# Performance work log

Measured on AMD Instinct MI355X. Metric: run time of the kernel, lower is better.

Reference implementation:

```python
import jax, jax.numpy as jnp
import numpy as np

GROUP = 16  # 4-bit quantization group size along in_features
LN_EPS = 1e-5


def dequant4bit(q, s):
    # q: [O, I] int32 values in [0, 15]; s: [O, I//GROUP] per-group absmax scales
    O, I = q.shape
    w = q.astype(jnp.float32) * (2.0 / 15.0) - 1.0          # map to [-1, 1]
    w = w.reshape(O, I // GROUP, GROUP) * s[:, :, None]      # per-group scale
    return w.reshape(O, I)


def qlora_linear(x, q, s, b, A, B):
    # base 4-bit dequantized matmul + bias
    w = dequant4bit(q, s)                                    # [O, I]
    base = x @ w.T + b                                       # [N, O]
    # LoRA low-rank delta; scaling = lora_alpha/lora_dim = 1.0
    delta = (x @ A.T) @ B.T                                  # [N, r] @ [r, O]
    return base + delta


def layernorm(x, g, b):
    m = jnp.mean(x, axis=-1, keepdims=True)
    v = jnp.mean((x - m) ** 2, axis=-1, keepdims=True)
    return (x - m) * jax.lax.rsqrt(v + LN_EPS) * g + b


def setup_inputs() -> dict:
    key = jax.random.key(0)
    ks = jax.random.split(key, 6)
    N, D, R, L, NB = 16384, 1024, 32, 18, 6  # tokens, dim, lora rank, num linears, num blocks
    x = jax.random.normal(ks[0], (N, D), dtype=jnp.float32)
    qw = jax.random.randint(ks[1], (L, D, D), 0, 16, dtype=jnp.int32)
    scales = jax.random.uniform(ks[2], (L, D, D // GROUP), dtype=jnp.float32) * 0.1
    bias = jax.random.normal(ks[3], (L, D), dtype=jnp.float32) * 0.02
    lora_A = jax.random.normal(ks[4], (L, R, D), dtype=jnp.float32) * 0.02
    lora_B = jax.random.normal(ks[5], (L, D, R), dtype=jnp.float32) * 0.02
    ln_g = jnp.ones((NB - 1, D), dtype=jnp.float32)
    ln_b = jnp.zeros((NB - 1, D), dtype=jnp.float32)
    return {"x": x, "qw": qw, "scales": scales, "bias": bias,
            "lora_A": lora_A, "lora_B": lora_B, "ln_g": ln_g, "ln_b": ln_b}


def reference(x, qw, scales, bias, lora_A, lora_B, ln_g, ln_b):
    n_blocks = 6
    for blk in range(n_blocks):
        h = x
        for j in range(3):
            li = 3 * blk + j
            h = qlora_linear(h, qw[li], scales[li], bias[li], lora_A[li], lora_B[li])
            if j < 2:
                h = jax.nn.relu(h)
        x = h + x  # residual
        if blk < n_blocks - 1:
            x = layernorm(x, ln_g[blk], ln_b[blk])
    return x
```

## Files before the change

kernel.cpp:

```cpp
#include <hip/hip_runtime.h>
#include <cstdint>


#define NTOK 16384
#define DIM  1024
#define KP   1088
#define RLORA 32
#define NLIN 18
#define NBLK 6

typedef unsigned short u16;
typedef __attribute__((ext_vector_type(8))) short short8;
typedef __attribute__((ext_vector_type(4))) float f32x4;

__device__ __forceinline__ u16 f2bf(float f) {
  uint32_t u = __float_as_uint(f);
  u += 0x7fffu + ((u >> 16) & 1u);
  return (u16)(u >> 16);
}
__device__ __forceinline__ float bf2f(u16 h) {
  return __uint_as_float(((uint32_t)h) << 16);
}
__device__ __forceinline__ void split_bf(float f, u16& h, u16& l) {
  h = f2bf(f);
  l = f2bf(f - bf2f(h));
}

__device__ __forceinline__ void gld16(const void* g, void* lds) {
  __builtin_amdgcn_global_load_lds(
      (const __attribute__((address_space(1))) uint32_t*)g,
      (__attribute__((address_space(3))) uint32_t*)lds, 16, 0, 0);
}


__global__ void pack_w_k(const int* __restrict__ qw, const float* __restrict__ sc,
                         const float* __restrict__ lb,
                         u16* __restrict__ Wh, u16* __restrict__ Wl) {
  const int idx = blockIdx.x * 256 + threadIdx.x;
  if (idx >= 1024 * (KP / 16)) return;
  const int g = idx % (KP / 16);
  const int o = idx / (KP / 16);
  u16 h[16], l[16];
  if (g < 64) {
    const int* q = qw + (size_t)o * 1024 + g * 16;
    const float s = sc[(size_t)o * 64 + g];
#pragma unroll
    for (int j = 0; j < 16; ++j) {
      float w = ((float)q[j] * (2.0f / 15.0f) - 1.0f) * s;
      split_bf(w, h[j], l[j]);
    }
  } else if (g < 66) {
    const float* B = lb + (size_t)o * RLORA + (g - 64) * 16;
#pragma unroll
    for (int j = 0; j < 16; ++j) split_bf(B[j], h[j], l[j]);
  } else {
#pragma unroll
    for (int j = 0; j < 16; ++j) { h[j] = 0; l[j] = 0; }
  }
  u16* wh = Wh + (size_t)o * KP + g * 16;
  u16* wl = Wl + (size_t)o * KP + g * 16;
#pragma unroll
  for (int j = 0; j < 16; ++j) { wh[j] = h[j]; wl[j] = l[j]; }
}

__global__ void pack_a_k(const float* __restrict__ la,
                         u16* __restrict__ Ah, u16* __restrict__ Al) {
  const int idx = blockIdx.x * 256 + threadIdx.x;
  if (idx >= NLIN * RLORA * (KP / 16)) return;
  const int g = idx % (KP / 16);
  const int rem = idx / (KP / 16);
  const int r = rem % RLORA, li = rem / RLORA;
  u16 h[16], l[16];
  if (g < 64) {
    const float* a = la + ((size_t)li * RLORA + r) * 1024 + g * 16;
#pragma unroll
    for (int j = 0; j < 16; ++j) split_bf(a[j], h[j], l[j]);
  } else {
#pragma unroll
    for (int j = 0; j < 16; ++j) { h[j] = 0; l[j] = 0; }
  }
  u16* ph = Ah + ((size_t)li * RLORA + r) * KP + g * 16;
  u16* pl = Al + ((size_t)li * RLORA + r) * KP + g * 16;
#pragma unroll
  for (int j = 0; j < 16; ++j) { ph[j] = h[j]; pl[j] = l[j]; }
}

__global__ void pack_x_k(const float* __restrict__ x,
                         u16* __restrict__ aAh, u16* __restrict__ aAl,
                         u16* __restrict__ aBh, u16* __restrict__ aBl) {
  const int idx = blockIdx.x * 256 + threadIdx.x;
  if (idx >= NTOK * (KP / 16)) return;
  const int g = idx % (KP / 16);
  const int n = idx / (KP / 16);
  const size_t dofs = (size_t)n * KP + g * 16;
  if (g < 64) {
    const float* xp = x + (size_t)n * DIM + g * 16;
#pragma unroll
    for (int j = 0; j < 16; ++j) {
      u16 h, l;
      split_bf(xp[j], h, l);
      aAh[dofs + j] = h; aAl[dofs + j] = l;
    }
  } else {
#pragma unroll
    for (int j = 0; j < 16; ++j) {
      aAh[dofs + j] = 0; aAl[dofs + j] = 0;
      aBh[dofs + j] = 0; aBl[dofs + j] = 0;
    }
  }
}

__global__ __launch_bounds__(256, 4) void t_k(
    u16* __restrict__ Xh, u16* __restrict__ Xl,
    const u16* __restrict__ LAh, const u16* __restrict__ LAl) {
  __shared__ __align__(16) u16 sXh[128 * 64], sXl[128 * 64];
  const int tid = threadIdx.x;
  const int lane = tid & 63, wave = tid >> 6;
  const int row0 = blockIdx.x * 128;

  f32x4 acc[2][2];
#pragma unroll
  for (int i = 0; i < 2; ++i)
#pragma unroll
    for (int j = 0; j < 2; ++j) acc[i][j] = {0.f, 0.f, 0.f, 0.f};

  const int sr = tid >> 3;
  const int ss = ((tid & 7) ^ (sr & 7)) * 8;
  const size_t xoff = (size_t)(row0 + sr) * KP + ss;
  const int arow = wave * 32 + (lane & 15);
  const int sl = lane >> 4, sx = lane & 7;

  for (int ks = 0; ks < 16; ++ks) {
    const int kofs = ks * 64;
#pragma unroll
    for (int r = 0; r < 4; ++r) {
      const size_t go = (size_t)(r * 32) * KP + kofs;
      const int lo = wave * 512 + r * 2048;
      gld16(Xh + xoff + go, &sXh[lo]);
      gld16(Xl + xoff + go, &sXl[lo]);
    }
    __syncthreads();
#pragma unroll
    for (int kk = 0; kk < 2; ++kk) {
      const int so = ((kk * 4 + sl) ^ sx) * 8;
      const int o0 = arow * 64 + so;
      const int o1 = (arow + 16) * 64 + so;
      short8 a0h = *(const short8*)&sXh[o0];
      short8 a0l = *(const short8*)&sXl[o0];
      short8 a1h = *(const short8*)&sXh[o1];
      short8 a1l = *(const short8*)&sXl[o1];
#pragma unroll
      for (int ni = 0; ni < 2; ++ni) {
        const int ar = ni * 16 + (lane & 15);
        const int ac = kofs + kk * 32 + sl * 8;
        short8 bh = *(const short8*)&LAh[(size_t)ar * KP + ac];
        short8 bl = *(const short8*)&LAl[(size_t)ar * KP + ac];
        f32x4 c = acc[0][ni];
        c = __builtin_amdgcn_mfma_f32_16x16x32_bf16(a0h, bl, c, 0, 0, 0);
        c = __builtin_amdgcn_mfma_f32_16x16x32_bf16(a0l, bh, c, 0, 0, 0);
        c = __builtin_amdgcn_mfma_f32_16x16x32_bf16(a0h, bh, c, 0, 0, 0);
        acc[0][ni] = c;
        c = acc[1][ni];
        c = __builtin_amdgcn_mfma_f32_16x16x32_bf16(a1h, bl, c, 0, 0, 0);
        c = __builtin_amdgcn_mfma_f32_16x16x32_bf16(a1l, bh, c, 0, 0, 0);
        c = __builtin_amdgcn_mfma_f32_16x16x32_bf16(a1h, bh, c, 0, 0, 0);
        acc[1][ni] = c;
      }
    }
    __syncthreads();
  }
  const int crow0 = row0 + wave * 32 + (lane >> 4) * 4;
#pragma unroll
  for (int ni = 0; ni < 2; ++ni) {
    const int col = DIM + ni * 16 + (lane & 15);
#pragma unroll
    for (int mi = 0; mi < 2; ++mi)
#pragma unroll
      for (int r = 0; r < 4; ++r) {
        const int rw = crow0 + mi * 16 + r;
        u16 h, l;
        split_bf(acc[mi][ni][r], h, l);
        Xh[(size_t)rw * KP + col] = h;
        Xl[(size_t)rw * KP + col] = l;
      }
  }
}

template <int MODE>
__global__ __launch_bounds__(256, 2) void gemm_k(
    const u16* __restrict__ Xh, const u16* __restrict__ Xl,
    const u16* __restrict__ Wh, const u16* __restrict__ Wl,
    const float* __restrict__ bias, const float* __restrict__ resid,
    float* __restrict__ outf, u16* __restrict__ Oh, u16* __restrict__ Ol) {
  __shared__ __align__(16) u16 sXh[128 * 64], sXl[128 * 64];
  __shared__ __align__(16) u16 sWh[128 * 64], sWl[128 * 64];
  const int tid = threadIdx.x;
  const int lane = tid & 63, wave = tid >> 6;
  const int wr = wave >> 1, wc = wave & 1;
  const int row0 = blockIdx.x * 128, col0 = blockIdx.y * 128;

  f32x4 acc[4][4];
#pragma unroll
  for (int i = 0; i < 4; ++i)
#pragma unroll
    for (int j = 0; j < 4; ++j) acc[i][j] = {0.f, 0.f, 0.f, 0.f};

  const int sr = tid >> 3;
  const int ss = ((tid & 7) ^ (sr & 7)) * 8;
  const size_t xoff = (size_t)(row0 + sr) * KP + ss;
  const size_t woff = (size_t)(col0 + sr) * KP + ss;

  const int arow = wr * 64 + (lane & 15);
  const int brow = wc * 64 + (lane & 15);
  const int sl = lane >> 4, sx = lane & 7;

  for (int ks = 0; ks < KP / 64; ++ks) {
    const int kofs = ks * 64;
#pragma unroll
    for (int r = 0; r < 4; ++r) {
      const size_t go = (size_t)(r * 32) * KP + kofs;
      const int lo = wave * 512 + r * 2048;
      gld16(Xh + xoff + go, &sXh[lo]);
      gld16(Xl + xoff + go, &sXl[lo]);
      gld16(Wh + woff + go, &sWh[lo]);
      gld16(Wl + woff + go, &sWl[lo]);
    }
    __syncthreads();
#pragma unroll
    for (int kk = 0; kk < 2; ++kk) {
      const int so = ((kk * 4 + sl) ^ sx) * 8;
      short8 ah[4], am[4], bh[4], bm[4];
#pragma unroll
      for (int mi = 0; mi < 4; ++mi) {
        const int off = (arow + mi * 16) * 64 + so;
        ah[mi] = *(const short8*)&sXh[off];
        am[mi] = *(const short8*)&sXl[off];
      }
#pragma unroll
      for (int ni = 0; ni < 4; ++ni) {
        const int off = (brow + ni * 16) * 64 + so;
        bh[ni] = *(const short8*)&sWh[off];
        bm[ni] = *(const short8*)&sWl[off];
      }
#pragma unroll
      for (int mi = 0; mi < 4; ++mi)
#pragma unroll
        for (int ni = 0; ni < 4; ++ni) {
          f32x4 c = acc[mi][ni];
          c = __builtin_amdgcn_mfma_f32_16x16x32_bf16(ah[mi], bm[ni], c, 0, 0, 0);
          c = __builtin_amdgcn_mfma_f32_16x16x32_bf16(am[mi], bh[ni], c, 0, 0, 0);
          c = __builtin_amdgcn_mfma_f32_16x16x32_bf16(ah[mi], bh[ni], c, 0, 0, 0);
          acc[mi][ni] = c;
        }
    }
    __syncthreads();
  }

  const int crow0 = row0 + wr * 64 + (lane >> 4) * 4;
  const int ccol0 = col0 + wc * 64 + (lane & 15);
#pragma unroll
  for (int ni = 0; ni < 4; ++ni) {
    const int col = ccol0 + ni * 16;
    const float bv = bias[col];
#pragma unroll
    for (int mi = 0; mi < 4; ++mi) {
#pragma unroll
      for (int r = 0; r < 4; ++r) {
        const int rw = crow0 + mi * 16 + r;
        float v = acc[mi][ni][r] + bv;
        if (MODE == 0) {
          v = fmaxf(v, 0.f);
          u16 h, l;
          split_bf(v, h, l);
          Oh[(size_t)rw * KP + col] = h;
          Ol[(size_t)rw * KP + col] = l;
        } else {
          v += resid[(size_t)rw * DIM + col];
          outf[(size_t)rw * DIM + col] = v;
        }
      }
    }
  }
}

__global__ __launch_bounds__(256) void ln_k(
    const float* __restrict__ y, const float* __restrict__ g,
    const float* __restrict__ b, float* __restrict__ ro,
    u16* __restrict__ Oh, u16* __restrict__ Ol) {
  const int row = blockIdx.x, tid = threadIdx.x;
  const int lane = tid & 63, wave = tid >> 6;
  __shared__ float r1[4], r2[4];
  const float4 v = ((const float4*)(y + (size_t)row * DIM))[tid];
  float s = v.x + v.y + v.z + v.w;
#pragma unroll
  for (int o = 32; o > 0; o >>= 1) s += __shfl_down(s, o);
  if (lane == 0) r1[wave] = s;
  __syncthreads();
  const float mean = (r1[0] + r1[1] + r1[2] + r1[3]) * (1.0f / DIM);
  const float d0 = v.x - mean, d1 = v.y - mean, d2 = v.z - mean, d3 = v.w - mean;
  float q = d0 * d0 + d1 * d1 + d2 * d2 + d3 * d3;
#pragma unroll
  for (int o = 32; o > 0; o >>= 1) q += __shfl_down(q, o);
  if (lane == 0) r2[wave] = q;
  __syncthreads();
  const float var = (r2[0] + r2[1] + r2[2] + r2[3]) * (1.0f / DIM);
  const float rs = rsqrtf(var + 1e-5f);
  const float4 gv = ((const float4*)g)[tid];
  const float4 bv = ((const float4*)b)[tid];
  const float o0 = d0 * rs * gv.x + bv.x;
  const float o1 = d1 * rs * gv.y + bv.y;
  const float o2 = d2 * rs * gv.z + bv.z;
  const float o3 = d3 * rs * gv.w + bv.w;
  ((float4*)(ro + (size_t)row * DIM))[tid] = make_float4(o0, o1, o2, o3);
  u16 h0, l0, h1, l1, h2, l2, h3, l3;
  split_bf(o0, h0, l0); split_bf(o1, h1, l1);
  split_bf(o2, h2, l2); split_bf(o3, h3, l3);
  ushort4 hh; hh.x = h0; hh.y = h1; hh.z = h2; hh.w = h3;
  ushort4 ll; ll.x = l0; ll.y = l1; ll.z = l2; ll.w = l3;
  *(ushort4*)&Oh[(size_t)row * KP + tid * 4] = hh;
  *(ushort4*)&Ol[(size_t)row * KP + tid * 4] = ll;
}

extern "C" void kernel_launch(void* const* d_in, const int* in_sizes, int n_in,
                              void* d_out, int out_size, void* d_ws, size_t ws_size,
                              hipStream_t stream) {
  const float* x      = (const float*)d_in[0];
  const int*   qw     = (const int*)d_in[1];
  const float* scales = (const float*)d_in[2];
  const float* bias   = (const float*)d_in[3];
  const float* lora_A = (const float*)d_in[4];
  const float* lora_B = (const float*)d_in[5];
  const float* ln_g   = (const float*)d_in[6];
  const float* ln_b   = (const float*)d_in[7];

  char* p = (char*)d_ws;
  auto carve = [&](size_t bytes) {
    char* r = p;
    p += (bytes + 255) & ~(size_t)255;
    return (void*)r;
  };
  u16* Wh  = (u16*)carve((size_t)1024 * KP * 2);
  u16* Wl  = (u16*)carve((size_t)1024 * KP * 2);
  u16* Ah  = (u16*)carve((size_t)NLIN * RLORA * KP * 2);
  u16* Al  = (u16*)carve((size_t)NLIN * RLORA * KP * 2);
  u16* aAh = (u16*)carve((size_t)NTOK * KP * 2);
  u16* aAl = (u16*)carve((size_t)NTOK * KP * 2);
  u16* aBh = (u16*)carve((size_t)NTOK * KP * 2);
  u16* aBl = (u16*)carve((size_t)NTOK * KP * 2);
  float* residb = (float*)carve((size_t)NTOK * DIM * 4);
  float* ybuf   = (float*)d_out;

  {
    const int tot = NLIN * RLORA * (KP / 16);
    pack_a_k<<<(tot + 255) / 256, 256, 0, stream>>>(lora_A, Ah, Al);
  }
  {
    const int tot = NTOK * (KP / 16);
    pack_x_k<<<(tot + 255) / 256, 256, 0, stream>>>(x, aAh, aAl, aBh, aBl);
  }

  u16 *inH = aAh, *inL = aAl, *outH = aBh, *outL = aBl;
  const float* resid = x;
  const int wtot = 1024 * (KP / 16);
  for (int blk = 0; blk < NBLK; ++blk) {
    for (int j = 0; j < 3; ++j) {
      const int li = 3 * blk + j;
      pack_w_k<<<(wtot + 255) / 256, 256, 0, stream>>>(
          qw + (size_t)li * DIM * DIM, scales + (size_t)li * DIM * (DIM / 16),
          lora_B + (size_t)li * DIM * RLORA, Wh, Wl);
      t_k<<<NTOK / 128, 256, 0, stream>>>(
          inH, inL, Ah + (size_t)li * RLORA * KP, Al + (size_t)li * RLORA * KP);
      const float* lb = bias + (size_t)li * DIM;
      dim3 grid(NTOK / 128, DIM / 128);
      if (j < 2) {
        gemm_k<0><<<grid, 256, 0, stream>>>(inH, inL, Wh, Wl, lb,
                                            nullptr, nullptr, outH, outL);
        u16* t;
        t = inH; inH = outH; outH = t;
        t = inL; inL = outL; outL = t;
      } else {
        gemm_k<1><<<grid, 256, 0, stream>>>(inH, inL, Wh, Wl, lb,
                                            resid, ybuf, nullptr, nullptr);
        if (blk < NBLK - 1) {
          ln_k<<<NTOK, 256, 0, stream>>>(ybuf, ln_g + (size_t)blk * DIM,
                                         ln_b + (size_t)blk * DIM, residb,
                                         outH, outL);
          resid = residb;
          u16* t;
          t = inH; inH = outH; outH = t;
          t = inL; inL = outL; outL = t;
        }
      }
    }
  }
  (void)in_sizes; (void)n_in; (void)out_size; (void)ws_size;
}
```

Before: 2.920 ms.

## Concatenate hi/lo split operands along K and use 256x256 pipelined GEMM

Activations and weights are re-laid out so the hi and lo bf16 halves are concatenated along K (X=[h|l], W=[h|l|h]), which turns the three-MFMA split-bf16 product into one long GEMM with K=3264. The main GEMM becomes a 512-thread, 256x256-tile kernel with double-buffered LDS, staggered global-to-LDS prefetch, s_setprio around MFMA phases and a swizzled block order. The LoRA t_k kernel likewise uses the concatenated layout with double buffering. The intent is more data reuse per tile and better overlap of loads with MFMAs. The cost is higher register and LDS pressure. The LoRA intermediate is now stored only as hi bf16, dropping its lo part, so precision is slightly reduced.

```diff
diff --git a/kernel.cpp b/kernel.cpp
--- a/kernel.cpp
+++ b/kernel.cpp
@@ -5,6 +5,9 @@
 #define NTOK 16384
 #define DIM  1024
 #define KP   1088
+#define KX   2176
+#define KC   3264
+#define NSTEP 51
 #define RLORA 32
 #define NLIN 18
 #define NBLK 6
@@ -25,255 +28,303 @@
   h = f2bf(f);
   l = f2bf(f - bf2f(h));
 }
-
 __device__ __forceinline__ void gld16(const void* g, void* lds) {
   __builtin_amdgcn_global_load_lds(
       (const __attribute__((address_space(1))) uint32_t*)g,
       (__attribute__((address_space(3))) uint32_t*)lds, 16, 0, 0);
 }
 
-
 __global__ void pack_w_k(const int* __restrict__ qw, const float* __restrict__ sc,
-                         const float* __restrict__ lb,
-                         u16* __restrict__ Wh, u16* __restrict__ Wl) {
+                         const float* __restrict__ lb, u16* __restrict__ Wc) {
   const int idx = blockIdx.x * 256 + threadIdx.x;
-  if (idx >= 1024 * (KP / 16)) return;
-  const int g = idx % (KP / 16);
-  const int o = idx / (KP / 16);
-  u16 h[16], l[16];
-  if (g < 64) {
+  if (idx >= 1024 * (KC / 16)) return;
+  const int c = idx % (KC / 16);
+  const int o = idx / (KC / 16);
+  int kind = 4, g = 0;
+  if      (c < 64)  { kind = 0; g = c; }
+  else if (c < 66)  { kind = 2; g = c - 64; }
+  else if (c < 68)  { kind = 4; }
+  else if (c < 132) { kind = 1; g = c - 68; }
+  else if (c < 134) { kind = 3; g = c - 132; }
+  else if (c < 136) { kind = 4; }
+  else if (c < 200) { kind = 0; g = c - 136; }
+  else if (c < 202) { kind = 2; g = c - 200; }
+  u16 out[16];
+  if (kind == 0 || kind == 1) {
     const int* q = qw + (size_t)o * 1024 + g * 16;
     const float s = sc[(size_t)o * 64 + g];
 #pragma unroll
     for (int j = 0; j < 16; ++j) {
       float w = ((float)q[j] * (2.0f / 15.0f) - 1.0f) * s;
-      split_bf(w, h[j], l[j]);
-    }
-  } else if (g < 66) {
-    const float* B = lb + (size_t)o * RLORA + (g - 64) * 16;
-#pragma unroll
-    for (int j = 0; j < 16; ++j) split_bf(B[j], h[j], l[j]);
+      u16 h, l; split_bf(w, h, l);
+      out[j] = (kind == 0) ? h : l;
+    }
+  } else if (kind == 2 || kind == 3) {
+    const float* B = lb + (size_t)o * RLORA + g * 16;
+#pragma unroll
+    for (int j = 0; j < 16; ++j) {
+      u16 h, l; split_bf(B[j], h, l);
+      out[j] = (kind == 2) ? h : l;
+    }
   } else {
 #pragma unroll
-    for (int j = 0; j < 16; ++j) { h[j] = 0; l[j] = 0; }
-  }
-  u16* wh = Wh + (size_t)o * KP + g * 16;
-  u16* wl = Wl + (size_t)o * KP + g * 16;
-#pragma unroll
-  for (int j = 0; j < 16; ++j) { wh[j] = h[j]; wl[j] = l[j]; }
-}
-
-__global__ void pack_a_k(const float* __restrict__ la,
-                         u16* __restrict__ Ah, u16* __restrict__ Al) {
+    for (int j = 0; j < 16; ++j) out[j] = 0;
+  }
+  u16* w = Wc + (size_t)o * KC + c * 16;
+#pragma unroll
+  for (int j = 0; j < 16; ++j) w[j] = out[j];
+}
+
+__global__ void pack_a_k(const float* __restrict__ la, u16* __restrict__ Ac) {
   const int idx = blockIdx.x * 256 + threadIdx.x;
-  if (idx >= NLIN * RLORA * (KP / 16)) return;
-  const int g = idx % (KP / 16);
-  const int rem = idx / (KP / 16);
-  const int r = rem % RLORA, li = rem / RLORA;
-  u16 h[16], l[16];
-  if (g < 64) {
-    const float* a = la + ((size_t)li * RLORA + r) * 1024 + g * 16;
-#pragma unroll
-    for (int j = 0; j < 16; ++j) split_bf(a[j], h[j], l[j]);
+  if (idx >= NLIN * RLORA * (KX / 16)) return;
+  const int c = idx % (KX / 16);
+  const int rr = idx / (KX / 16);
+  u16 out[16];
+  int kind = 2, g = 0;
+  if (c < 64) { kind = 0; g = c; }
+  else if (c >= 68 && c < 132) { kind = 1; g = c - 68; }
+  if (kind < 2) {
+    const float* a = la + (size_t)rr * 1024 + g * 16;
+#pragma unroll
+    for (int j = 0; j < 16; ++j) {
+      u16 h, l; split_bf(a[j], h, l);
+      out[j] = (kind == 0) ? h : l;
+    }
   } else {
 #pragma unroll
-    for (int j = 0; j < 16; ++j) { h[j] = 0; l[j] = 0; }
-  }
-  u16* ph = Ah + ((size_t)li * RLORA + r) * KP + g * 16;
-  u16* pl = Al + ((size_t)li * RLORA + r) * KP + g * 16;
-#pragma unroll
-  for (int j = 0; j < 16; ++j) { ph[j] = h[j]; pl[j] = l[j]; }
+    for (int j = 0; j < 16; ++j) out[j] = 0;
+  }
+  u16* p = Ac + (size_t)rr * KX + c * 16;
+#pragma unroll
+  for (int j = 0; j < 16; ++j) p[j] = out[j];
 }
 
 __global__ void pack_x_k(const float* __restrict__ x,
-                         u16* __restrict__ aAh, u16* __restrict__ aAl,
-                         u16* __restrict__ aBh, u16* __restrict__ aBl) {
+                         u16* __restrict__ aA, u16* __restrict__ aB) {
   const int idx = blockIdx.x * 256 + threadIdx.x;
-  if (idx >= NTOK * (KP / 16)) return;
-  const int g = idx % (KP / 16);
-  const int n = idx / (KP / 16);
-  const size_t dofs = (size_t)n * KP + g * 16;
-  if (g < 64) {
-    const float* xp = x + (size_t)n * DIM + g * 16;
+  if (idx >= NTOK * 68) return;
+  const int c = idx % 68;
+  const int n = idx / 68;
+  const size_t base = (size_t)n * KX;
+  if (c < 64) {
+    const float* xp = x + (size_t)n * DIM + c * 16;
 #pragma unroll
     for (int j = 0; j < 16; ++j) {
-      u16 h, l;
-      split_bf(xp[j], h, l);
-      aAh[dofs + j] = h; aAl[dofs + j] = l;
+      u16 h, l; split_bf(xp[j], h, l);
+      aA[base + c * 16 + j] = h;
+      aA[base + KP + c * 16 + j] = l;
     }
   } else {
 #pragma unroll
     for (int j = 0; j < 16; ++j) {
-      aAh[dofs + j] = 0; aAl[dofs + j] = 0;
-      aBh[dofs + j] = 0; aBl[dofs + j] = 0;
+      aA[base + c * 16 + j] = 0;      aA[base + KP + c * 16 + j] = 0;
+      aB[base + c * 16 + j] = 0;      aB[base + KP + c * 16 + j] = 0;
     }
   }
 }
 
 __global__ __launch_bounds__(256, 4) void t_k(
-    u16* __restrict__ Xh, u16* __restrict__ Xl,
-    const u16* __restrict__ LAh, const u16* __restrict__ LAl) {
-  __shared__ __align__(16) u16 sXh[128 * 64], sXl[128 * 64];
+    u16* __restrict__ X, const u16* __restrict__ Ac) {
+  __shared__ __align__(16) u16 sX[2][128 * 64];
+  const int tid = threadIdx.x, lane = tid & 63, wave = tid >> 6;
+  const int row0 = blockIdx.x * 128;
+  const int srow = tid >> 3;
+  const int lslot = ((tid & 7) ^ (srow & 7)) * 8;
+  const int fr = lane & 15, sl = lane >> 4, sx = lane & 7;
+
+  f32x4 acc[2][2];
+#pragma unroll
+  for (int i = 0; i < 2; ++i)
+#pragma unroll
+    for (int j = 0; j < 2; ++j) acc[i][j] = {0.f, 0.f, 0.f, 0.f};
+
+  auto stage = [&](int buf, int s) {
+    const int xb = (s < 17 ? s : s - 17) * 64;
+#pragma unroll
+    for (int i = 0; i < 4; ++i)
+      gld16(X + (size_t)(row0 + i * 32 + srow) * KX + xb + lslot,
+            &sX[buf][i * 2048 + wave * 512]);
+  };
+  stage(0, 0);
+  for (int t = 0; t < 34; ++t) {
+    const int c = t & 1;
+    if (t + 1 < 34) {
+      stage(c ^ 1, t + 1);
+      asm volatile("s_waitcnt vmcnt(4)" ::: "memory");
+    } else {
+      asm volatile("s_waitcnt vmcnt(0)" ::: "memory");
+    }
+    __builtin_amdgcn_s_barrier();
+    short8 av[2][2], bv[2][2];
+#pragma unroll
+    for (int mi = 0; mi < 2; ++mi)
+#pragma unroll
+      for (int kk = 0; kk < 2; ++kk) {
+        const int row = wave * 32 + mi * 16 + fr;
+        av[mi][kk] = *(const short8*)&sX[c][row * 64 + (((kk * 4 + sl) ^ sx)) * 8];
+      }
+#pragma unroll
+    for (int ni = 0; ni < 2; ++ni)
+#pragma unroll
+      for (int kk = 0; kk < 2; ++kk) {
+        const int ar = ni * 16 + fr;
+        bv[ni][kk] = *(const short8*)&Ac[(size_t)ar * KX + t * 64 + kk * 32 + sl * 8];
+      }
+#pragma unroll
+    for (int mi = 0; mi < 2; ++mi)
+#pragma unroll
+      for (int ni = 0; ni < 2; ++ni)
+#pragma unroll
+        for (int kk = 0; kk < 2; ++kk)
+          acc[mi][ni] = __builtin_amdgcn_mfma_f32_16x16x32_bf16(
+              av[mi][kk], bv[ni][kk], acc[mi][ni], 0, 0, 0);
+    __builtin_amdgcn_s_barrier();
+  }
+  const int crow0 = row0 + wave * 32 + (lane >> 4) * 4;
+#pragma unroll
+  for (int ni = 0; ni < 2; ++ni) {
+    const int col = DIM + ni * 16 + fr;
+#pragma unroll
+    for (int mi = 0; mi < 2; ++mi)
+#pragma unroll
+      for (int r = 0; r < 4; ++r)
+        X[(size_t)(crow0 + mi * 16 + r) * KX + col] = f2bf(acc[mi][ni][r]);
+  }
+}
+
+#define READ_A(Q)                                                           \
+  short8 aa0[2], aa1[2];                                                    \
+  {                                                                         \
+    const int r0 = (wr * 128 + ((Q) * 2 + 0) * 16 + fr) * 64;               \
+    const int r1 = (wr * 128 + ((Q) * 2 + 1) * 16 + fr) * 64;               \
+    aa0[0] = *(const short8*)&sA[c][r0 + ((0 + sl) ^ sx) * 8];              \
+    aa0[1] = *(const short8*)&sA[c][r0 + ((4 + sl) ^ sx) * 8];              \
+    aa1[0] = *(const short8*)&sA[c][r1 + ((0 + sl) ^ sx) * 8];              \
+    aa1[1] = *(const short8*)&sA[c][r1 + ((4 + sl) ^ sx) * 8];              \
+  }
+
+#define PHASE_TAIL(Q)                                                       \
+  __builtin_amdgcn_s_barrier();                                             \
+  asm volatile("s_waitcnt lgkmcnt(0)" ::: "memory");                        \
+  __builtin_amdgcn_s_setprio(1);                                            \
+  _Pragma("unroll")                                                         \
+  for (int kk = 0; kk < 2; ++kk) {                                          \
+    _Pragma("unroll")                                                       \
+    for (int ni = 0; ni < 4; ++ni) {                                        \
+      acc[(Q) * 2 + 0][ni] = __builtin_amdgcn_mfma_f32_16x16x32_bf16(       \
+          aa0[kk], b[ni][kk], acc[(Q) * 2 + 0][ni], 0, 0, 0);               \
+      acc[(Q) * 2 + 1][ni] = __builtin_amdgcn_mfma_f32_16x16x32_bf16(       \
+          aa1[kk], b[ni][kk], acc[(Q) * 2 + 1][ni], 0, 0, 0);               \
+    }                                                                       \
+  }                                                                         \
+  __builtin_amdgcn_s_setprio(0);                                            \
+  __builtin_amdgcn_s_barrier();
+
+template <int MODE>
+__global__ __launch_bounds__(512, 2) void gemm8_k(
+    const u16* __restrict__ X, const u16* __restrict__ W,
+    const float* __restrict__ bias, const float* __restrict__ resid,
+    float* __restrict__ outf, u16* __restrict__ O) {
+  __shared__ __align__(16) u16 sA[2][256 * 64];
+  __shared__ __align__(16) u16 sB[2][256 * 64];
   const int tid = threadIdx.x;
   const int lane = tid & 63, wave = tid >> 6;
-  const int row0 = blockIdx.x * 128;
-
-  f32x4 acc[2][2];
-#pragma unroll
-  for (int i = 0; i < 2; ++i)
-#pragma unroll
-    for (int j = 0; j < 2; ++j) acc[i][j] = {0.f, 0.f, 0.f, 0.f};
-
-  const int sr = tid >> 3;
-  const int ss = ((tid & 7) ^ (sr & 7)) * 8;
-  const size_t xoff = (size_t)(row0 + sr) * KP + ss;
-  const int arow = wave * 32 + (lane & 15);
-  const int sl = lane >> 4, sx = lane & 7;
-
-  for (int ks = 0; ks < 16; ++ks) {
-    const int kofs = ks * 64;
-#pragma unroll
-    for (int r = 0; r < 4; ++r) {
-      const size_t go = (size_t)(r * 32) * KP + kofs;
-      const int lo = wave * 512 + r * 2048;
-      gld16(Xh + xoff + go, &sXh[lo]);
-      gld16(Xl + xoff + go, &sXl[lo]);
-    }
-    __syncthreads();
-#pragma unroll
-    for (int kk = 0; kk < 2; ++kk) {
-      const int so = ((kk * 4 + sl) ^ sx) * 8;
-      const int o0 = arow * 64 + so;
-      const int o1 = (arow + 16) * 64 + so;
-      short8 a0h = *(const short8*)&sXh[o0];
-      short8 a0l = *(const short8*)&sXl[o0];
-      short8 a1h = *(const short8*)&sXh[o1];
-      short8 a1l = *(const short8*)&sXl[o1];
-#pragma unroll
-      for (int ni = 0; ni < 2; ++ni) {
-        const int ar = ni * 16 + (lane & 15);
-        const int ac = kofs + kk * 32 + sl * 8;
-        short8 bh = *(const short8*)&LAh[(size_t)ar * KP + ac];
-        short8 bl = *(const short8*)&LAl[(size_t)ar * KP + ac];
-        f32x4 c = acc[0][ni];
-        c = __builtin_amdgcn_mfma_f32_16x16x32_bf16(a0h, bl, c, 0, 0, 0);
-        c = __builtin_amdgcn_mfma_f32_16x16x32_bf16(a0l, bh, c, 0, 0, 0);
-        c = __builtin_amdgcn_mfma_f32_16x16x32_bf16(a0h, bh, c, 0, 0, 0);
-        acc[0][ni] = c;
-        c = acc[1][ni];
-        c = __builtin_amdgcn_mfma_f32_16x16x32_bf16(a1h, bl, c, 0, 0, 0);
-        c = __builtin_amdgcn_mfma_f32_16x16x32_bf16(a1l, bh, c, 0, 0, 0);
-        c = __builtin_amdgcn_mfma_f32_16x16x32_bf16(a1h, bh, c, 0, 0, 0);
-        acc[1][ni] = c;
+  const int wr = wave >> 2, wc = wave & 3;
+
+  const int flat = blockIdx.y * 64 + blockIdx.x;
+  const int fl2 = (flat & 7) * 32 + (flat >> 3);
+  const int row0 = (fl2 & 63) * 256;
+  const int col0 = (fl2 >> 6) * 256;
+
+  const int srow = tid >> 3;
+  const int lslot = ((tid & 7) ^ (srow & 7)) * 8;
+  const int fr = lane & 15, sl = lane >> 4, sx = lane & 7;
+
+  f32x4 acc[8][4];
+#pragma unroll
+  for (int i = 0; i < 8; ++i)
+#pragma unroll
+    for (int j = 0; j < 4; ++j) acc[i][j] = {0.f, 0.f, 0.f, 0.f};
+
+  auto xbase = [](int s) {
+    return s < 17 ? s * 64 : (s < 34 ? (s - 17) * 64 : KP + (s - 34) * 64);
+  };
+  auto stX = [&](int buf, int s, int i) {
+    gld16(X + (size_t)(row0 + i * 64 + srow) * KX + xbase(s) + lslot,
+          &sA[buf][i * 4096 + wave * 512]);
+  };
+  auto stW = [&](int buf, int s, int i) {
+    gld16(W + (size_t)(col0 + i * 64 + srow) * KC + s * 64 + lslot,
+          &sB[buf][i * 4096 + wave * 512]);
+  };
+
+#pragma unroll
+  for (int i = 0; i < 4; ++i) stX(0, 0, i);
+#pragma unroll
+  for (int i = 0; i < 4; ++i) stW(0, 0, i);
+#pragma unroll
+  for (int i = 0; i < 4; ++i) stW(1, 1, i);
+  stX(1, 1, 0);
+  stX(1, 1, 2);
+  asm volatile("s_waitcnt vmcnt(6)" ::: "memory");
+  __builtin_amdgcn_s_barrier();
+
+  for (int t = 0; t < NSTEP; ++t) {
+    const int c = t & 1;
+    const bool h1 = (t + 1 < NSTEP), h2 = (t + 2 < NSTEP);
+    short8 b[4][2];
+#pragma unroll
+    for (int ni = 0; ni < 4; ++ni) {
+      const int row = (wc * 64 + ni * 16 + fr) * 64;
+#pragma unroll
+      for (int kk = 0; kk < 2; ++kk)
+        b[ni][kk] = *(const short8*)&sB[c][row + ((kk * 4 + sl) ^ sx) * 8];
+    }
+    {
+      READ_A(0)
+      if (h1) { stX(c ^ 1, t + 1, 1); stX(c ^ 1, t + 1, 3); }
+      PHASE_TAIL(0)
+    }
+    {
+      READ_A(1)
+      if (h2) { stW(c, t + 2, 0); stW(c, t + 2, 1); }
+      PHASE_TAIL(1)
+    }
+    {
+      READ_A(2)
+      if (h2) { stW(c, t + 2, 2); stW(c, t + 2, 3); stX(c, t + 2, 0); }
+      PHASE_TAIL(2)
+    }
+    {
+      READ_A(3)
+      if (h2) {
+        stX(c, t + 2, 2);
+        asm volatile("s_waitcnt vmcnt(6)" ::: "memory");
+      } else if (h1) {
+        asm volatile("s_waitcnt vmcnt(0)" ::: "memory");
       }
-    }
-    __syncthreads();
-  }
-  const int crow0 = row0 + wave * 32 + (lane >> 4) * 4;
-#pragma unroll
-  for (int ni = 0; ni < 2; ++ni) {
-    const int col = DIM + ni * 16 + (lane & 15);
-#pragma unroll
-    for (int mi = 0; mi < 2; ++mi)
+      PHASE_TAIL(3)
+    }
+  }
+
+  const int crow0 = row0 + wr * 128 + (lane >> 4) * 4;
+  const int ccolb = col0 + wc * 64 + fr;
+#pragma unroll
+  for (int ni = 0; ni < 4; ++ni) {
+    const int col = ccolb + ni * 16;
+    const float bvv = bias[col];
+#pragma unroll
+    for (int mi = 0; mi < 8; ++mi) {
 #pragma unroll
       for (int r = 0; r < 4; ++r) {
         const int rw = crow0 + mi * 16 + r;
-        u16 h, l;
-        split_bf(acc[mi][ni][r], h, l);
-        Xh[(size_t)rw * KP + col] = h;
-        Xl[(size_t)rw * KP + col] = l;
-      }
-  }
-}
-
-template <int MODE>
-__global__ __launch_bounds__(256, 2) void gemm_k(
-    const u16* __restrict__ Xh, const u16* __restrict__ Xl,
-    const u16* __restrict__ Wh, const u16* __restrict__ Wl,
-    const float* __restrict__ bias, const float* __restrict__ resid,
-    float* __restrict__ outf, u16* __restrict__ Oh, u16* __restrict__ Ol) {
-  __shared__ __align__(16) u16 sXh[128 * 64], sXl[128 * 64];
-  __shared__ __align__(16) u16 sWh[128 * 64], sWl[128 * 64];
-  const int tid = threadIdx.x;
-  const int lane = tid & 63, wave = tid >> 6;
-  const int wr = wave >> 1, wc = wave & 1;
-  const int row0 = blockIdx.x * 128, col0 = blockIdx.y * 128;
-
-  f32x4 acc[4][4];
-#pragma unroll
-  for (int i = 0; i < 4; ++i)
-#pragma unroll
-    for (int j = 0; j < 4; ++j) acc[i][j] = {0.f, 0.f, 0.f, 0.f};
-
-  const int sr = tid >> 3;
-  const int ss = ((tid & 7) ^ (sr & 7)) * 8;
-  const size_t xoff = (size_t)(row0 + sr) * KP + ss;
-  const size_t woff = (size_t)(col0 + sr) * KP + ss;
-
-  const int arow = wr * 64 + (lane & 15);
-  const int brow = wc * 64 + (lane & 15);
-  const int sl = lane >> 4, sx = lane & 7;
-
-  for (int ks = 0; ks < KP / 64; ++ks) {
-    const int kofs = ks * 64;
-#pragma unroll
-    for (int r = 0; r < 4; ++r) {
-      const size_t go = (size_t)(r * 32) * KP + kofs;
-      const int lo = wave * 512 + r * 2048;
-      gld16(Xh + xoff + go, &sXh[lo]);
-      gld16(Xl + xoff + go, &sXl[lo]);
-      gld16(Wh + woff + go, &sWh[lo]);
-      gld16(Wl + woff + go, &sWl[lo]);
-    }
-    __syncthreads();
-#pragma unroll
-    for (int kk = 0; kk < 2; ++kk) {
-      const int so = ((kk * 4 + sl) ^ sx) * 8;
-      short8 ah[4], am[4], bh[4], bm[4];
-#pragma unroll
-      for (int mi = 0; mi < 4; ++mi) {
-        const int off = (arow + mi * 16) * 64 + so;
-        ah[mi] = *(const short8*)&sXh[off];
-        am[mi] = *(const short8*)&sXl[off];
-      }
-#pragma unroll
-      for (int ni = 0; ni < 4; ++ni) {
-        const int off = (brow + ni * 16) * 64 + so;
-        bh[ni] = *(const short8*)&sWh[off];
-        bm[ni] = *(const short8*)&sWl[off];
-      }
-#pragma unroll
-      for (int mi = 0; mi < 4; ++mi)
-#pragma unroll
-        for (int ni = 0; ni < 4; ++ni) {
-          f32x4 c = acc[mi][ni];
-          c = __builtin_amdgcn_mfma_f32_16x16x32_bf16(ah[mi], bm[ni], c, 0, 0, 0);
-          c = __builtin_amdgcn_mfma_f32_16x16x32_bf16(am[mi], bh[ni], c, 0, 0, 0);
-          c = __builtin_amdgcn_mfma_f32_16x16x32_bf16(ah[mi], bh[ni], c, 0, 0, 0);
-          acc[mi][ni] = c;
-        }
-    }
-    __syncthreads();
-  }
-
-  const int crow0 = row0 + wr * 64 + (lane >> 4) * 4;
-  const int ccol0 = col0 + wc * 64 + (lane & 15);
-#pragma unroll
-  for (int ni = 0; ni < 4; ++ni) {
-    const int col = ccol0 + ni * 16;
-    const float bv = bias[col];
-#pragma unroll
-    for (int mi = 0; mi < 4; ++mi) {
-#pragma unroll
-      for (int r = 0; r < 4; ++r) {
-        const int rw = crow0 + mi * 16 + r;
-        float v = acc[mi][ni][r] + bv;
+        float v = acc[mi][ni][r] + bvv;
         if (MODE == 0) {
           v = fmaxf(v, 0.f);
-          u16 h, l;
-          split_bf(v, h, l);
-          Oh[(size_t)rw * KP + col] = h;
-          Ol[(size_t)rw * KP + col] = l;
+          u16 h, l; split_bf(v, h, l);
+          O[(size_t)rw * KX + col] = h;
+          O[(size_t)rw * KX + KP + col] = l;
         } else {
           v += resid[(size_t)rw * DIM + col];
           outf[(size_t)rw * DIM + col] = v;
@@ -285,8 +336,7 @@
 
 __global__ __launch_bounds__(256) void ln_k(
     const float* __restrict__ y, const float* __restrict__ g,
-    const float* __restrict__ b, float* __restrict__ ro,
-    u16* __restrict__ Oh, u16* __restrict__ Ol) {
+    const float* __restrict__ b, float* __restrict__ ro, u16* __restrict__ O) {
   const int row = blockIdx.x, tid = threadIdx.x;
   const int lane = tid & 63, wave = tid >> 6;
   __shared__ float r1[4], r2[4];
@@ -317,8 +367,8 @@
   split_bf(o2, h2, l2); split_bf(o3, h3, l3);
   ushort4 hh; hh.x = h0; hh.y = h1; hh.z = h2; hh.w = h3;
   ushort4 ll; ll.x = l0; ll.y = l1; ll.z = l2; ll.w = l3;
-  *(ushort4*)&Oh[(size_t)row * KP + tid * 4] = hh;
-  *(ushort4*)&Ol[(size_t)row * KP + tid * 4] = ll;
+  *(ushort4*)&O[(size_t)row * KX + tid * 4] = hh;
+  *(ushort4*)&O[(size_t)row * KX + KP + tid * 4] = ll;
 }
 
 extern "C" void kernel_launch(void* const* d_in, const int* in_sizes, int n_in,
@@ -339,56 +389,44 @@
     p += (bytes + 255) & ~(size_t)255;
     return (void*)r;
   };
-  u16* Wh  = (u16*)carve((size_t)1024 * KP * 2);
-  u16* Wl  = (u16*)carve((size_t)1024 * KP * 2);
-  u16* Ah  = (u16*)carve((size_t)NLIN * RLORA * KP * 2);
-  u16* Al  = (u16*)carve((size_t)NLIN * RLORA * KP * 2);
-  u16* aAh = (u16*)carve((size_t)NTOK * KP * 2);
-  u16* aAl = (u16*)carve((size_t)NTOK * KP * 2);
-  u16* aBh = (u16*)carve((size_t)NTOK * KP * 2);
-  u16* aBl = (u16*)carve((size_t)NTOK * KP * 2);
+  u16* Wc  = (u16*)carve((size_t)1024 * KC * 2);
+  u16* Ac  = (u16*)carve((size_t)NLIN * RLORA * KX * 2);
+  u16* aA  = (u16*)carve((size_t)NTOK * KX * 2);
+  u16* aB  = (u16*)carve((size_t)NTOK * KX * 2);
   float* residb = (float*)carve((size_t)NTOK * DIM * 4);
   float* ybuf   = (float*)d_out;
 
   {
-    const int tot = NLIN * RLORA * (KP / 16);
-    pack_a_k<<<(tot + 255) / 256, 256, 0, stream>>>(lora_A, Ah, Al);
+    const int tot = NLIN * RLORA * (KX / 16);
+    pack_a_k<<<(tot + 255) / 256, 256, 0, stream>>>(lora_A, Ac);
   }
   {
-    const int tot = NTOK * (KP / 16);
-    pack_x_k<<<(tot + 255) / 256, 256, 0, stream>>>(x, aAh, aAl, aBh, aBl);
-  }
-
-  u16 *inH = aAh, *inL = aAl, *outH = aBh, *outL = aBl;
+    const int tot = NTOK * 68;
+    pack_x_k<<<(tot + 255) / 256, 256, 0, stream>>>(x, aA, aB);
+  }
+
+  u16 *inA = aA, *outA = aB;
   const float* resid = x;
-  const int wtot = 1024 * (KP / 16);
+  const int wtot = 1024 * (KC / 16);
+  dim3 grid(64, 4);
   for (int blk = 0; blk < NBLK; ++blk) {
     for (int j = 0; j < 3; ++j) {
       const int li = 3 * blk + j;
       pack_w_k<<<(wtot + 255) / 256, 256, 0, stream>>>(
           qw + (size_t)li * DIM * DIM, scales + (size_t)li * DIM * (DIM / 16),
-          lora_B + (size_t)li * DIM * RLORA, Wh, Wl);
-      t_k<<<NTOK / 128, 256, 0, stream>>>(
-          inH, inL, Ah + (size_t)li * RLORA * KP, Al + (size_t)li * RLORA * KP);
+          lora_B + (size_t)li * DIM * RLORA, Wc);
+      t_k<<<NTOK / 128, 256, 0, stream>>>(inA, Ac + (size_t)li * RLORA * KX);
       const float* lb = bias + (size_t)li * DIM;
-      dim3 grid(NTOK / 128, DIM / 128);
       if (j < 2) {
-        gemm_k<0><<<grid, 256, 0, stream>>>(inH, inL, Wh, Wl, lb,
-                                            nullptr, nullptr, outH, outL);
-        u16* t;
-        t = inH; inH = outH; outH = t;
-        t = inL; inL = outL; outL = t;
+        gemm8_k<0><<<grid, 512, 0, stream>>>(inA, Wc, lb, nullptr, nullptr, outA);
+        u16* tswp = inA; inA = outA; outA = tswp;
       } else {
-        gemm_k<1><<<grid, 256, 0, stream>>>(inH, inL, Wh, Wl, lb,
-                                            resid, ybuf, nullptr, nullptr);
+        gemm8_k<1><<<grid, 512, 0, stream>>>(inA, Wc, lb, resid, ybuf, nullptr);
         if (blk < NBLK - 1) {
           ln_k<<<NTOK, 256, 0, stream>>>(ybuf, ln_g + (size_t)blk * DIM,
-                                         ln_b + (size_t)blk * DIM, residb,
-                                         outH, outL);
+                                         ln_b + (size_t)blk * DIM, residb, outA);
           resid = residb;
-          u16* t;
-          t = inH; inH = outH; outH = t;
-          t = inL; inL = outL; outL = t;
+          u16* tswp = inA; inA = outA; outA = tswp;
         }
       }
     }
```

Result: slower. 3.680 ms (+26.0%).

## Slim LoRA projection kernel to bf16-hi input and remap GEMM blocks per XCD

Applied to the files above, without the earlier changes.

The LoRA down-projection kernel now loads only the high bf16 half of the activations, uses 64-row tiles with two MFMAs per step instead of three, and writes only the high part of the projected result. This cuts shared memory, traffic and MFMA work in that kernel, at some cost in precision in the LoRA path. The main GEMM remaps its flat block index so blocks on the same XCD share row panels and all column tiles, aiming for better L2 reuse. The pack_a index math is also simplified.

```diff
diff --git a/kernel.cpp b/kernel.cpp
--- a/kernel.cpp
+++ b/kernel.cpp
@@ -69,18 +69,17 @@
   if (idx >= NLIN * RLORA * (KP / 16)) return;
   const int g = idx % (KP / 16);
   const int rem = idx / (KP / 16);
-  const int r = rem % RLORA, li = rem / RLORA;
   u16 h[16], l[16];
   if (g < 64) {
-    const float* a = la + ((size_t)li * RLORA + r) * 1024 + g * 16;
+    const float* a = la + (size_t)rem * 1024 + g * 16;
 #pragma unroll
     for (int j = 0; j < 16; ++j) split_bf(a[j], h[j], l[j]);
   } else {
 #pragma unroll
     for (int j = 0; j < 16; ++j) { h[j] = 0; l[j] = 0; }
   }
-  u16* ph = Ah + ((size_t)li * RLORA + r) * KP + g * 16;
-  u16* pl = Al + ((size_t)li * RLORA + r) * KP + g * 16;
+  u16* ph = Ah + (size_t)rem * KP + g * 16;
+  u16* pl = Al + (size_t)rem * KP + g * 16;
 #pragma unroll
   for (int j = 0; j < 16; ++j) { ph[j] = h[j]; pl[j] = l[j]; }
 }
@@ -111,78 +110,52 @@
 }
 
 __global__ __launch_bounds__(256, 4) void t_k(
-    u16* __restrict__ Xh, u16* __restrict__ Xl,
-    const u16* __restrict__ LAh, const u16* __restrict__ LAl) {
-  __shared__ __align__(16) u16 sXh[128 * 64], sXl[128 * 64];
-  const int tid = threadIdx.x;
-  const int lane = tid & 63, wave = tid >> 6;
-  const int row0 = blockIdx.x * 128;
-
-  f32x4 acc[2][2];
-#pragma unroll
-  for (int i = 0; i < 2; ++i)
-#pragma unroll
-    for (int j = 0; j < 2; ++j) acc[i][j] = {0.f, 0.f, 0.f, 0.f};
-
-  const int sr = tid >> 3;
-  const int ss = ((tid & 7) ^ (sr & 7)) * 8;
-  const size_t xoff = (size_t)(row0 + sr) * KP + ss;
-  const int arow = wave * 32 + (lane & 15);
-  const int sl = lane >> 4, sx = lane & 7;
-
-  for (int ks = 0; ks < 16; ++ks) {
-    const int kofs = ks * 64;
-#pragma unroll
-    for (int r = 0; r < 4; ++r) {
-      const size_t go = (size_t)(r * 32) * KP + kofs;
-      const int lo = wave * 512 + r * 2048;
-      gld16(Xh + xoff + go, &sXh[lo]);
-      gld16(Xl + xoff + go, &sXl[lo]);
-    }
+    u16* __restrict__ Xh, const u16* __restrict__ LAh,
+    const u16* __restrict__ LAl) {
+  __shared__ __align__(16) u16 sX[64 * 64];
+  const int tid = threadIdx.x, lane = tid & 63, wave = tid >> 6;
+  const int row0 = blockIdx.x * 64;
+  const int fr = lane & 15, sl = lane >> 4;
+  const int xr = tid >> 3, xs = tid & 7;
+
+  f32x4 acc[2];
+  acc[0] = {0.f, 0.f, 0.f, 0.f};
+  acc[1] = {0.f, 0.f, 0.f, 0.f};
+
+  for (int t = 0; t < 16; ++t) {
+    const int kofs = t * 64;
+    gld16(Xh + (size_t)(row0 + xr) * KP + kofs + (xs ^ (xr & 7)) * 8,
+          &sX[tid * 8]);
+    gld16(Xh + (size_t)(row0 + 32 + xr) * KP + kofs + (xs ^ (xr & 7)) * 8,
+          &sX[2048 + tid * 8]);
     __syncthreads();
+    short8 a[2];
 #pragma unroll
     for (int kk = 0; kk < 2; ++kk) {
-      const int so = ((kk * 4 + sl) ^ sx) * 8;
-      const int o0 = arow * 64 + so;
-      const int o1 = (arow + 16) * 64 + so;
-      short8 a0h = *(const short8*)&sXh[o0];
-      short8 a0l = *(const short8*)&sXl[o0];
-      short8 a1h = *(const short8*)&sXh[o1];
-      short8 a1l = *(const short8*)&sXl[o1];
-#pragma unroll
-      for (int ni = 0; ni < 2; ++ni) {
-        const int ar = ni * 16 + (lane & 15);
+      const int arow = wave * 16 + fr;
+      a[kk] = *(const short8*)&sX[arow * 64 + (((kk * 4 + sl) ^ (fr & 7))) * 8];
+    }
+#pragma unroll
+    for (int n = 0; n < 2; ++n) {
+      const int ar = n * 16 + fr;
+#pragma unroll
+      for (int kk = 0; kk < 2; ++kk) {
         const int ac = kofs + kk * 32 + sl * 8;
         short8 bh = *(const short8*)&LAh[(size_t)ar * KP + ac];
         short8 bl = *(const short8*)&LAl[(size_t)ar * KP + ac];
-        f32x4 c = acc[0][ni];
-        c = __builtin_amdgcn_mfma_f32_16x16x32_bf16(a0h, bl, c, 0, 0, 0);
-        c = __builtin_amdgcn_mfma_f32_16x16x32_bf16(a0l, bh, c, 0, 0, 0);
-        c = __builtin_amdgcn_mfma_f32_16x16x32_bf16(a0h, bh, c, 0, 0, 0);
-        acc[0][ni] = c;
-        c = acc[1][ni];
-        c = __builtin_amdgcn_mfma_f32_16x16x32_bf16(a1h, bl, c, 0, 0, 0);
-        c = __builtin_amdgcn_mfma_f32_16x16x32_bf16(a1l, bh, c, 0, 0, 0);
-        c = __builtin_amdgcn_mfma_f32_16x16x32_bf16(a1h, bh, c, 0, 0, 0);
-        acc[1][ni] = c;
+        acc[n] = __builtin_amdgcn_mfma_f32_16x16x32_bf16(a[kk], bh, acc[n], 0, 0, 0);
+        acc[n] = __builtin_amdgcn_mfma_f32_16x16x32_bf16(a[kk], bl, acc[n], 0, 0, 0);
       }
     }
     __syncthreads();
   }
-  const int crow0 = row0 + wave * 32 + (lane >> 4) * 4;
-#pragma unroll
-  for (int ni = 0; ni < 2; ++ni) {
-    const int col = DIM + ni * 16 + (lane & 15);
-#pragma unroll
-    for (int mi = 0; mi < 2; ++mi)
-#pragma unroll
-      for (int r = 0; r < 4; ++r) {
-        const int rw = crow0 + mi * 16 + r;
-        u16 h, l;
-        split_bf(acc[mi][ni][r], h, l);
-        Xh[(size_t)rw * KP + col] = h;
-        Xl[(size_t)rw * KP + col] = l;
-      }
+  const int crow0 = row0 + wave * 16 + (lane >> 4) * 4;
+#pragma unroll
+  for (int n = 0; n < 2; ++n) {
+    const int col = DIM + n * 16 + fr;
+#pragma unroll
+    for (int r = 0; r < 4; ++r)
+      Xh[(size_t)(crow0 + r) * KP + col] = f2bf(acc[n][r]);
   }
 }
 
@@ -197,7 +170,11 @@
   const int tid = threadIdx.x;
   const int lane = tid & 63, wave = tid >> 6;
   const int wr = wave >> 1, wc = wave & 1;
-  const int row0 = blockIdx.x * 128, col0 = blockIdx.y * 128;
+
+  const int flat = blockIdx.y * 128 + blockIdx.x;
+  const int xcd = flat & 7, idx = flat >> 3;
+  const int row0 = (xcd * 16 + (idx >> 3)) * 128;
+  const int col0 = (idx & 7) * 128;
 
   f32x4 acc[4][4];
 #pragma unroll
@@ -368,10 +345,10 @@
       pack_w_k<<<(wtot + 255) / 256, 256, 0, stream>>>(
           qw + (size_t)li * DIM * DIM, scales + (size_t)li * DIM * (DIM / 16),
           lora_B + (size_t)li * DIM * RLORA, Wh, Wl);
-      t_k<<<NTOK / 128, 256, 0, stream>>>(
-          inH, inL, Ah + (size_t)li * RLORA * KP, Al + (size_t)li * RLORA * KP);
+      t_k<<<NTOK / 64, 256, 0, stream>>>(
+          inH, Ah + (size_t)li * RLORA * KP, Al + (size_t)li * RLORA * KP);
       const float* lb = bias + (size_t)li * DIM;
-      dim3 grid(NTOK / 128, DIM / 128);
+      dim3 grid(128, 8);
       if (j < 2) {
         gemm_k<0><<<grid, 256, 0, stream>>>(inH, inL, Wh, Wl, lb,
                                             nullptr, nullptr, outH, outL);
```

New measurement: 2.887 ms. About the same (-1.1%).
